# Performance work log

Hardware: AMD Instinct MI355X
Metric: run time of the kernel (lower is better)

Reference implementation:

```python
import jax, jax.numpy as jnp
import numpy as np

B, Q, NC = 32, 1024, 256  # batch, queries, classes incl. background slot
IOU_THR = 0.5


def setup_inputs() -> dict:
    key = jax.random.key(0)
    k1, k2, k3 = jax.random.split(key, 3)
    pred_logits = jax.random.normal(k1, (B, Q, NC), dtype=jnp.float32)
    pred_boxes = jax.random.uniform(k2, (B, Q, 4), dtype=jnp.float32)  # cxcywh in [0,1]
    target_sizes = jax.random.randint(k3, (B, 2), 0, 1333)  # (h, w) per image
    return {"pred_logits": pred_logits, "pred_boxes": pred_boxes, "target_sizes": target_sizes}


def box_cxcywh_to_xyxy(b):
    cx, cy, w, h = jnp.split(b, 4, axis=-1)
    return jnp.concatenate([cx - 0.5 * w, cy - 0.5 * h, cx + 0.5 * w, cy + 0.5 * h], axis=-1)


def pairwise_iou(boxes):
    # boxes: [Q,4] in xyxy
    area = (boxes[:, 2] - boxes[:, 0]) * (boxes[:, 3] - boxes[:, 1])
    lt = jnp.maximum(boxes[:, None, :2], boxes[None, :, :2])
    rb = jnp.minimum(boxes[:, None, 2:], boxes[None, :, 2:])
    wh = jnp.clip(rb - lt, 0.0)
    inter = wh[..., 0] * wh[..., 1]
    union = area[:, None] + area[None, :] - inter
    return inter / jnp.maximum(union, 1e-9)


def greedy_nms(boxes, scores, iou_thr):
    # Class-agnostic greedy NMS (matches torchvision.ops.nms semantics);
    # returns a boolean keep mask over the original query order.
    n = scores.shape[0]
    order = jnp.argsort(-scores)
    iou = pairwise_iou(boxes[order])  # [Q,Q] on score-sorted boxes
    idx = jnp.arange(n)

    def body(i, keep):
        # if box i is still kept, suppress all lower-scored boxes with IoU > thr
        sup = keep[i] & (iou[i] > iou_thr) & (idx > i)
        return keep & ~sup

    keep_sorted = jax.lax.fori_loop(0, n, body, jnp.ones((n,), dtype=bool))
    return jnp.zeros((n,), dtype=bool).at[order].set(keep_sorted)


def reference(pred_logits, pred_boxes, target_sizes):
    prob = jax.nn.softmax(pred_logits, axis=-1)
    fg = prob[..., :-1]  # drop background class
    scores = fg.max(axis=-1)  # [B,Q]
    labels = fg.argmax(axis=-1)  # [B,Q]

    boxes = box_cxcywh_to_xyxy(pred_boxes)  # [B,Q,4]
    img_h = target_sizes[:, 0].astype(boxes.dtype)
    img_w = target_sizes[:, 1].astype(boxes.dtype)
    scale_fct = jnp.stack([img_w, img_h, img_w, img_h], axis=1)  # [B,4]
    boxes = boxes * scale_fct[:, None, :]

    # use_nms=True path: keep mask instead of data-dependent gather (jit-safe)
    keep = jax.vmap(greedy_nms, in_axes=(0, 0, None))(boxes, scores, IOU_THR)  # [B,Q] bool
    return scores, labels, boxes, keep
```

## Files before the change

### kernel.cpp

```cpp
#include <hip/hip_runtime.h>


constexpr int kB  = 32;
constexpr int kQ  = 1024;
constexpr int kNC = 256;
constexpr int kBQ = kB * kQ;

typedef unsigned long long u64;
typedef unsigned int u32;

__device__ __forceinline__ bool iou_gt(const float4& a, float aa,
                                       const float4& b, float ba) {
  float lx = fmaxf(a.x, b.x);
  float ly = fmaxf(a.y, b.y);
  float rx = fminf(a.z, b.z);
  float ry = fminf(a.w, b.w);
  float w  = fmaxf(__fsub_rn(rx, lx), 0.0f);
  float h  = fmaxf(__fsub_rn(ry, ly), 0.0f);
  float inter = __fmul_rn(w, h);
  float u  = fmaxf(__fsub_rn(__fadd_rn(aa, ba), inter), 1e-9f);
  return (double)inter > (double)u * 0.50000002980232238769531250;
}

__global__ void k_score_box(const float* __restrict__ logits,
                            const float* __restrict__ pboxes,
                            const int* __restrict__ ts,
                            float* __restrict__ out,
                            u64* __restrict__ keys) {
  int gw   = (int)((blockIdx.x * blockDim.x + threadIdx.x) >> 6);
  int lane = (int)(threadIdx.x & 63);
  if (gw >= kBQ) return;

  float4 v = reinterpret_cast<const float4*>(logits)[gw * (kNC / 4) + lane];

  float fw = (lane == 63) ? -INFINITY : v.w;
  float fm = v.x; int fi = lane * 4;
  if (v.y > fm) { fm = v.y; fi = lane * 4 + 1; }
  if (v.z > fm) { fm = v.z; fi = lane * 4 + 2; }
  if (fw  > fm) { fm = fw;  fi = lane * 4 + 3; }
  for (int off = 32; off > 0; off >>= 1) {
    float om = __shfl_xor(fm, off, 64);
    int   oi = __shfl_xor(fi, off, 64);
    if (om > fm || (om == fm && oi < fi)) { fm = om; fi = oi; }
  }

  float last = __shfl(v.w, 63, 64);
  float m = fmaxf(fm, last);

  float s = expf(v.x - m) + expf(v.y - m) + expf(v.z - m) + expf(v.w - m);
  for (int off = 32; off > 0; off >>= 1) s += __shfl_xor(s, off, 64);

  if (lane == 0) {
    float sc = expf(fm - m) / s;
    out[gw]       = sc;
    out[kBQ + gw] = (float)fi;
    keys[gw] = ((u64)(~__float_as_uint(sc)) << 32) | (u32)(gw & (kQ - 1));

    float4 pb = reinterpret_cast<const float4*>(pboxes)[gw];
    int bi = gw >> 10;
    float ih = (float)ts[bi * 2 + 0];
    float iw = (float)ts[bi * 2 + 1];
    float hw = __fmul_rn(0.5f, pb.z);
    float hh = __fmul_rn(0.5f, pb.w);
    float x0 = __fmul_rn(__fsub_rn(pb.x, hw), iw);
    float y0 = __fmul_rn(__fsub_rn(pb.y, hh), ih);
    float x1 = __fmul_rn(__fadd_rn(pb.x, hw), iw);
    float y1 = __fmul_rn(__fadd_rn(pb.y, hh), ih);
    reinterpret_cast<float4*>(out + 2 * kBQ)[gw] = make_float4(x0, y0, x1, y1);
  }
}

__global__ void __launch_bounds__(256) k_rank(const u64* __restrict__ keys,
                                              const float* __restrict__ out,
                                              u32* __restrict__ order,
                                              float4* __restrict__ sbox,
                                              float* __restrict__ sarea) {
  __shared__ u64 ks[kQ];
  const int b = (int)blockIdx.x, sb = (int)blockIdx.y, tid = (int)threadIdx.x;

  for (int t = tid; t < kQ; t += 256) ks[t] = keys[b * kQ + t];
  __syncthreads();

  const int j = sb * 256 + tid;
  const u64 kj = ks[j];
  int cnt = 0;
  #pragma unroll 8
  for (int k = 0; k < kQ; ++k) cnt += (int)(ks[k] < kj);

  float4 bx = reinterpret_cast<const float4*>(out + 2 * kBQ)[b * kQ + j];
  order[b * kQ + cnt] = (u32)j;
  sbox[b * kQ + cnt]  = bx;
  sarea[b * kQ + cnt] = __fmul_rn(__fsub_rn(bx.z, bx.x), __fsub_rn(bx.w, bx.y));
}

__global__ void __launch_bounds__(256) k_mask(const float4* __restrict__ sbox,
                                              const float* __restrict__ sarea,
                                              u64* __restrict__ maskT) {
  const int b = (int)blockIdx.x;
  const int wv = (int)(threadIdx.x >> 6), lane = (int)(threadIdx.x & 63);
  const int r = (int)blockIdx.y * 4 + wv;

  int jb = (int)((sqrtf((float)(8 * r + 1)) - 1.0f) * 0.5f);
  while ((jb + 1) * (jb + 2) / 2 <= r) ++jb;
  while (jb * (jb + 1) / 2 > r) --jb;
  const int c = r - jb * (jb + 1) / 2;

  __shared__ float4 iboxS[4][64];
  __shared__ float  iareaS[4][64];
  iboxS[wv][lane]  = sbox[b * kQ + c * 64 + lane];
  iareaS[wv][lane] = sarea[b * kQ + c * 64 + lane];

  const int j = jb * 64 + lane;
  const float4 bj = sbox[b * kQ + j];
  const float  aj = sarea[b * kQ + j];

  u32 wlo = 0, whi = 0;
  if (c < jb) {
    #pragma unroll 4
    for (int l = 0; l < 32; ++l)
      wlo |= ((u32)iou_gt(iboxS[wv][l], iareaS[wv][l], bj, aj)) << l;
    #pragma unroll 4
    for (int l = 0; l < 32; ++l)
      whi |= ((u32)iou_gt(iboxS[wv][l + 32], iareaS[wv][l + 32], bj, aj)) << l;
  } else {
    #pragma unroll 4
    for (int l = 0; l < 32; ++l)
      wlo |= ((u32)((l < lane) && iou_gt(iboxS[wv][l], iareaS[wv][l], bj, aj))) << l;
    #pragma unroll 4
    for (int l = 0; l < 32; ++l)
      whi |= ((u32)((l + 32 < lane) && iou_gt(iboxS[wv][l + 32], iareaS[wv][l + 32], bj, aj))) << l;
  }
  maskT[(b * 16 + c) * kQ + j] = ((u64)whi << 32) | wlo;
}

__global__ void __launch_bounds__(1024) k_scan(const u64* __restrict__ maskT,
                                               const u32* __restrict__ order,
                                               float* __restrict__ out) {
  __shared__ u64 aliveS[16];
  __shared__ u32 doneS;
  const int b = (int)blockIdx.x, tid = (int)threadIdx.x;
  const int lane = tid & 63, k = tid >> 6;

  const u64* mb = maskT + (size_t)(b * 16) * kQ;
  u64 w[15];
  #pragma unroll
  for (int c = 0; c < 15; ++c)
    w[c] = (c < k) ? mb[c * kQ + k * 64 + lane] : 0ull;
  u64 d = mb[k * kQ + k * 64 + lane];
  u32 oj = order[b * kQ + k * 64 + lane];

  if (tid == 0) doneS = 0;
  __syncthreads();

  bool supp = false;
  #pragma unroll
  for (int c = 0; c < 15; ++c) {
    if (c >= k) break;
    u32 dn;
    do {
      dn = __hip_atomic_load(&doneS, __ATOMIC_ACQUIRE, __HIP_MEMORY_SCOPE_WORKGROUP);
    } while ((int)dn <= c);
    supp = supp || ((w[c] & aliveS[c]) != 0ull);
  }

  u64 dead     = __ballot(supp);
  u64 alive    = 0ull;
  u64 resolved = dead;
  for (int it = 0; it < 64 && resolved != ~0ull; ++it) {
    u64 nA = __ballot((d & ~dead) == 0ull) & ~resolved;
    alive    |= nA;
    resolved |= nA;
    u64 nD = __ballot((d & alive) != 0ull) & ~resolved;
    dead     |= nD;
    resolved |= nD;
  }
  if (lane == 0) {
    aliveS[k] = alive;
    __hip_atomic_store(&doneS, (u32)(k + 1), __ATOMIC_RELEASE, __HIP_MEMORY_SCOPE_WORKGROUP);
  }

  out[6 * kBQ + b * kQ + (int)oj] = ((alive >> lane) & 1ull) ? 1.0f : 0.0f;
}

extern "C" void kernel_launch(void* const* d_in, const int* in_sizes, int n_in,
                              void* d_out, int out_size, void* d_ws, size_t ws_size,
                              hipStream_t stream) {
  const float* logits = (const float*)d_in[0];
  const float* pboxes = (const float*)d_in[1];
  const int*   ts     = (const int*)d_in[2];
  float* out = (float*)d_out;

  char* ws = (char*)d_ws;
  u64*    maskT = (u64*)ws;
  u32*    order = (u32*)(ws + (4 << 20));
  float4* sbox  = (float4*)(ws + (4 << 20) + (128 << 10));
  float*  sarea = (float*)(ws + (4 << 20) + (640 << 10));
  u64*    keys  = (u64*)(ws + (4 << 20) + (768 << 10));

  dim3 g1(kBQ / 4), t1(256);
  k_score_box<<<g1, t1, 0, stream>>>(logits, pboxes, ts, out, keys);

  dim3 g2(kB, kQ / 256), t2(256);
  k_rank<<<g2, t2, 0, stream>>>(keys, out, order, sbox, sarea);

  dim3 g3(kB, 34), t3(256);
  k_mask<<<g3, t3, 0, stream>>>(sbox, sarea, maskT);

  k_scan<<<kB, 1024, 0, stream>>>(maskT, order, out);
}
```

Before: 59.17 us.

## Fuse mask and scan kernels via global counter; broadcast rank keys with readlane

Merges the IoU mask kernel and the greedy scan kernel into one launch. Nine blocks per image build the triangular mask tiles and bump a per-image atomic counter, and a tenth block spins on that counter before running the scan. This removes one kernel launch and its boundary. In the rank kernel, each lane now loads a pair of keys from LDS and the comparison loop broadcasts them with readlane instead of reading every key from LDS per thread. The spin-wait assumes that the scan blocks never occupy the GPU in a way that starves the producer blocks, which is a forward-progress risk.

```diff
diff --git a/kernel.cpp b/kernel.cpp
--- a/kernel.cpp
+++ b/kernel.cpp
@@ -74,18 +74,33 @@
                                               const float* __restrict__ out,
                                               u32* __restrict__ order,
                                               float4* __restrict__ sbox,
-                                              float* __restrict__ sarea) {
-  __shared__ u64 ks[kQ];
+                                              float* __restrict__ sarea,
+                                              u32* __restrict__ done) {
+  __shared__ __align__(16) u64 ks[kQ];
   const int b = (int)blockIdx.x, sb = (int)blockIdx.y, tid = (int)threadIdx.x;
+  if (sb == 0 && tid == 0) done[b] = 0;
 
   for (int t = tid; t < kQ; t += 256) ks[t] = keys[b * kQ + t];
   __syncthreads();
 
+  const int lane = tid & 63;
   const int j = sb * 256 + tid;
   const u64 kj = ks[j];
   int cnt = 0;
-  #pragma unroll 8
-  for (int k = 0; k < kQ; ++k) cnt += (int)(ks[k] < kj);
+  const ulonglong2* ks2 = reinterpret_cast<const ulonglong2*>(ks);
+  for (int bi = 0; bi < 8; ++bi) {
+    ulonglong2 kk = ks2[bi * 64 + lane];
+    int a0lo = (int)(u32)kk.x, a0hi = (int)(u32)(kk.x >> 32);
+    int a1lo = (int)(u32)kk.y, a1hi = (int)(u32)(kk.y >> 32);
+    #pragma unroll 8
+    for (int l = 0; l < 64; ++l) {
+      u64 k0 = ((u64)(u32)__builtin_amdgcn_readlane(a0hi, l) << 32)
+             |  (u64)(u32)__builtin_amdgcn_readlane(a0lo, l);
+      u64 k1 = ((u64)(u32)__builtin_amdgcn_readlane(a1hi, l) << 32)
+             |  (u64)(u32)__builtin_amdgcn_readlane(a1lo, l);
+      cnt += (int)(k0 < kj) + (int)(k1 < kj);
+    }
+  }
 
   float4 bx = reinterpret_cast<const float4*>(out + 2 * kBQ)[b * kQ + j];
   order[b * kQ + cnt] = (u32)j;
@@ -93,54 +108,66 @@
   sarea[b * kQ + cnt] = __fmul_rn(__fsub_rn(bx.z, bx.x), __fsub_rn(bx.w, bx.y));
 }
 
-__global__ void __launch_bounds__(256) k_mask(const float4* __restrict__ sbox,
-                                              const float* __restrict__ sarea,
-                                              u64* __restrict__ maskT) {
-  const int b = (int)blockIdx.x;
-  const int wv = (int)(threadIdx.x >> 6), lane = (int)(threadIdx.x & 63);
-  const int r = (int)blockIdx.y * 4 + wv;
-
-  int jb = (int)((sqrtf((float)(8 * r + 1)) - 1.0f) * 0.5f);
-  while ((jb + 1) * (jb + 2) / 2 <= r) ++jb;
-  while (jb * (jb + 1) / 2 > r) --jb;
-  const int c = r - jb * (jb + 1) / 2;
-
-  __shared__ float4 iboxS[4][64];
-  __shared__ float  iareaS[4][64];
-  iboxS[wv][lane]  = sbox[b * kQ + c * 64 + lane];
-  iareaS[wv][lane] = sarea[b * kQ + c * 64 + lane];
-
-  const int j = jb * 64 + lane;
-  const float4 bj = sbox[b * kQ + j];
-  const float  aj = sarea[b * kQ + j];
-
-  u32 wlo = 0, whi = 0;
-  if (c < jb) {
-    #pragma unroll 4
-    for (int l = 0; l < 32; ++l)
-      wlo |= ((u32)iou_gt(iboxS[wv][l], iareaS[wv][l], bj, aj)) << l;
-    #pragma unroll 4
-    for (int l = 0; l < 32; ++l)
-      whi |= ((u32)iou_gt(iboxS[wv][l + 32], iareaS[wv][l + 32], bj, aj)) << l;
-  } else {
-    #pragma unroll 4
-    for (int l = 0; l < 32; ++l)
-      wlo |= ((u32)((l < lane) && iou_gt(iboxS[wv][l], iareaS[wv][l], bj, aj))) << l;
-    #pragma unroll 4
-    for (int l = 0; l < 32; ++l)
-      whi |= ((u32)((l + 32 < lane) && iou_gt(iboxS[wv][l + 32], iareaS[wv][l + 32], bj, aj))) << l;
-  }
-  maskT[(b * 16 + c) * kQ + j] = ((u64)whi << 32) | wlo;
-}
-
-__global__ void __launch_bounds__(1024) k_scan(const u64* __restrict__ maskT,
-                                               const u32* __restrict__ order,
-                                               float* __restrict__ out) {
+__global__ void __launch_bounds__(1024) k_mask_scan(const float4* __restrict__ sbox,
+                                                    const float* __restrict__ sarea,
+                                                    u64* __restrict__ maskT,
+                                                    const u32* __restrict__ order,
+                                                    u32* __restrict__ done,
+                                                    float* __restrict__ out) {
+  const int b = (int)blockIdx.x, y = (int)blockIdx.y;
+  const int tid = (int)threadIdx.x, lane = tid & 63, wv = tid >> 6;
+
+  __shared__ float4 iboxS[16][64];
+  __shared__ float  iareaS[16][64];
   __shared__ u64 aliveS[16];
   __shared__ u32 doneS;
-  const int b = (int)blockIdx.x, tid = (int)threadIdx.x;
-  const int lane = tid & 63, k = tid >> 6;
-
+
+  if (y < 9) {
+    const int r = y * 16 + wv;
+    if (r < 136) {
+      int jb = (int)((sqrtf((float)(8 * r + 1)) - 1.0f) * 0.5f);
+      while ((jb + 1) * (jb + 2) / 2 <= r) ++jb;
+      while (jb * (jb + 1) / 2 > r) --jb;
+      const int c = r - jb * (jb + 1) / 2;
+
+      iboxS[wv][lane]  = sbox[b * kQ + c * 64 + lane];
+      iareaS[wv][lane] = sarea[b * kQ + c * 64 + lane];
+
+      const int j = jb * 64 + lane;
+      const float4 bj = sbox[b * kQ + j];
+      const float  aj = sarea[b * kQ + j];
+
+      u32 wlo = 0, whi = 0;
+      if (c < jb) {
+        #pragma unroll 4
+        for (int l = 0; l < 32; ++l)
+          wlo |= ((u32)iou_gt(iboxS[wv][l], iareaS[wv][l], bj, aj)) << l;
+        #pragma unroll 4
+        for (int l = 0; l < 32; ++l)
+          whi |= ((u32)iou_gt(iboxS[wv][l + 32], iareaS[wv][l + 32], bj, aj)) << l;
+      } else {
+        #pragma unroll 4
+        for (int l = 0; l < 32; ++l)
+          wlo |= ((u32)((l < lane) && iou_gt(iboxS[wv][l], iareaS[wv][l], bj, aj))) << l;
+        #pragma unroll 4
+        for (int l = 0; l < 32; ++l)
+          whi |= ((u32)((l + 32 < lane) && iou_gt(iboxS[wv][l + 32], iareaS[wv][l + 32], bj, aj))) << l;
+      }
+      maskT[(b * 16 + c) * kQ + j] = ((u64)whi << 32) | wlo;
+    }
+    __syncthreads();
+    if (tid == 0)
+      __hip_atomic_fetch_add(&done[b], 1u, __ATOMIC_RELEASE, __HIP_MEMORY_SCOPE_AGENT);
+    return;
+  }
+
+  if (tid == 0) {
+    while (__hip_atomic_load(&done[b], __ATOMIC_ACQUIRE, __HIP_MEMORY_SCOPE_AGENT) < 9u)
+      __builtin_amdgcn_s_sleep(4);
+  }
+  __syncthreads();
+
+  const int k = wv;
   const u64* mb = maskT + (size_t)(b * 16) * kQ;
   u64 w[15];
   #pragma unroll
@@ -196,15 +223,14 @@
   float4* sbox  = (float4*)(ws + (4 << 20) + (128 << 10));
   float*  sarea = (float*)(ws + (4 << 20) + (640 << 10));
   u64*    keys  = (u64*)(ws + (4 << 20) + (768 << 10));
+  u32*    done  = (u32*)(ws + (4 << 20) + (1024 << 10));
 
   dim3 g1(kBQ / 4), t1(256);
   k_score_box<<<g1, t1, 0, stream>>>(logits, pboxes, ts, out, keys);
 
   dim3 g2(kB, kQ / 256), t2(256);
-  k_rank<<<g2, t2, 0, stream>>>(keys, out, order, sbox, sarea);
-
-  dim3 g3(kB, 34), t3(256);
-  k_mask<<<g3, t3, 0, stream>>>(sbox, sarea, maskT);
-
-  k_scan<<<kB, 1024, 0, stream>>>(maskT, order, out);
-}
+  k_rank<<<g2, t2, 0, stream>>>(keys, out, order, sbox, sarea, done);
+
+  dim3 g3(kB, 10), t3(1024);
+  k_mask_scan<<<g3, t3, 0, stream>>>(sbox, sarea, maskT, order, done, out);
+}
```

New measurement: 67.52 us. 1.14x slower.
